# Kernel tuning notes

Hardware: AMD Instinct MI355X
Metric: run time of the kernel (lower is better)

Reference implementation:

```python
import jax, jax.numpy as jnp
import numpy as np

N, P, E, D, OUT = 4096, 2048, 65536, 1024, 128


def _lin(k, fin, fout):
    kw, kb = jax.random.split(k)
    s = 1.0 / np.sqrt(fin)
    return (jax.random.uniform(kw, (fin, fout), jnp.float32, -s, s),
            jax.random.uniform(kb, (fout,), jnp.float32, -s, s))


def setup_inputs() -> dict:
    key = jax.random.key(0)
    ks = jax.random.split(key, 16)
    inst_feat = jax.random.normal(ks[0], (N, D), jnp.float32)
    phra_feat = jax.random.normal(ks[1], (P, D), jnp.float32)
    # unique (subject, object) pairs: the original overwrites duplicates in connection_marker
    pair_ids = jax.random.choice(ks[2], N * N, (E,), replace=False)
    conn_mat = jnp.stack([pair_ids // N, pair_ids % N]).astype(jnp.int32)  # [2, E]
    # every phrase id appears -> exist_phra_id == arange(P), matching original indexing
    phra_clu_idx = jax.random.permutation(ks[3], jnp.arange(E, dtype=jnp.int32) % P)
    p_s_W, p_s_b = _lin(ks[4], 2 * D, OUT)
    s_p_W, s_p_b = _lin(ks[5], 2 * D, OUT)
    p_o_W, p_o_b = _lin(ks[6], 2 * D, OUT)
    o_p_W, o_p_b = _lin(ks[7], 2 * D, OUT)
    inst_w1_W, inst_w1_b = _lin(ks[8], D, D)
    inst_w2_W, inst_w2_b = _lin(ks[9], D, D)
    phra_w1_W, phra_w1_b = _lin(ks[10], D, D)
    phra_w2_W, phra_w2_b = _lin(ks[11], D, D)
    return dict(inst_feat=inst_feat, phra_feat=phra_feat, conn_mat=conn_mat,
                phra_clu_idx=phra_clu_idx,
                p_s_W=p_s_W, p_s_b=p_s_b, p_o_W=p_o_W, p_o_b=p_o_b,
                o_p_W=o_p_W, o_p_b=o_p_b, s_p_W=s_p_W, s_p_b=s_p_b,
                inst_w1_W=inst_w1_W, inst_w1_b=inst_w1_b,
                inst_w2_W=inst_w2_W, inst_w2_b=inst_w2_b,
                phra_w1_W=phra_w1_W, phra_w1_b=phra_w1_b,
                phra_w2_W=phra_w2_W, phra_w2_b=phra_w2_b)


def _gated_msg(src, tgt, W, b):
    # MassageGenerator: gate = sigmoid(relu([src; tgt] @ W + b)).mean(1); msg = src * gate
    gate = jax.nn.sigmoid(jax.nn.relu(jnp.concatenate([src, tgt], axis=1) @ W + b)).mean(axis=1)
    return src * gate[:, None]


def _seg_mean(x, seg, num_segments):
    s = jax.ops.segment_sum(x, seg, num_segments=num_segments)
    c = jax.ops.segment_sum(jnp.ones((x.shape[0],), x.dtype), seg, num_segments=num_segments)
    return s / jnp.maximum(c, 1.0)[:, None]  # zeros where no edges == padded msg


def _refine(msg, tar, w1_W, w1_b, w2_W, w2_b):
    # MassageApply: out = input1 + relu(w1(input1)) + relu(w2(input2)); input1 = summed msg
    return msg + jax.nn.relu(msg @ w1_W + w1_b) + jax.nn.relu(tar @ w2_W + w2_b)


def reference(inst_feat, phra_feat, conn_mat, phra_clu_idx,
              p_s_W, p_s_b, p_o_W, p_o_b, o_p_W, o_p_b, s_p_W, s_p_b,
              inst_w1_W, inst_w1_b, inst_w2_W, inst_w2_b,
              phra_w1_W, phra_w1_b, phra_w2_W, phra_w2_b):
    s_idx, o_idx = conn_mat[0], conn_mat[1]
    subj_f = inst_feat[s_idx]          # [E, D]
    obj_f = inst_feat[o_idx]           # [E, D]
    phr_f = phra_feat[phra_clu_idx]    # [E, D]
    n, p = inst_feat.shape[0], phra_feat.shape[0]
    # phrase -> subject / object messages, mean over each node's incident edges
    p_s = _seg_mean(_gated_msg(phr_f, subj_f, p_s_W, p_s_b), s_idx, n)
    p_o = _seg_mean(_gated_msg(phr_f, obj_f, p_o_W, p_o_b), o_idx, n)
    # object / subject -> phrase messages, mean over edges sharing a cluster id
    o_p = _seg_mean(_gated_msg(obj_f, phr_f, o_p_W, o_p_b), phra_clu_idx, p)
    s_p = _seg_mean(_gated_msg(subj_f, phr_f, s_p_W, s_p_b), phra_clu_idx, p)
    inst_out = _refine((p_o + p_s) * 0.5, inst_feat, inst_w1_W, inst_w1_b, inst_w2_W, inst_w2_b)
    phra_out = _refine((o_p + s_p) * 0.5, phra_feat, phra_w1_W, phra_w1_b, phra_w2_W, phra_w2_b)
    return inst_out, phra_out
```

## Files before the change

### kernel.cpp

```cpp
#include <hip/hip_runtime.h>
#include <math.h>

constexpr int NN  = 4096;
constexpr int PP  = 2048;
constexpr int EE  = 65536;
constexpr int DD  = 1024;
constexpr int OUTF = 128;
constexpr int G4  = 512;

typedef __attribute__((ext_vector_type(8))) short short8v;
typedef __attribute__((ext_vector_type(4))) float f32x4;

__device__ __forceinline__ float sigmoid_relu(float z) {
    z = fmaxf(z, 0.0f);
    return 1.0f / (1.0f + __expf(-z));
}
__device__ __forceinline__ float b2f(ushort u) {
    return __uint_as_float(((unsigned int)u) << 16);
}
__device__ __forceinline__ ushort f2b(float f) {
    unsigned int x = __float_as_uint(f);
    return (ushort)((x + 0x7fffu + ((x >> 16) & 1u)) >> 16);
}
__device__ __forceinline__ unsigned int pack2(float a, float b) {
    return (unsigned int)f2b(a) | ((unsigned int)f2b(b) << 16);
}
__device__ __forceinline__ float lo16(unsigned int u) { return __uint_as_float(u << 16); }
__device__ __forceinline__ float hi16(unsigned int u) { return __uint_as_float(u & 0xffff0000u); }

#define GLD16(gptr, lptr) \
    __builtin_amdgcn_global_load_lds((__attribute__((address_space(1))) const void*)(gptr), \
                                     (__attribute__((address_space(3))) void*)(lptr), 16, 0, 0)
#define ASM_VMCNT(n) asm volatile("s_waitcnt vmcnt(" #n ")" ::: "memory")
#define BARRIER() do { asm volatile("" ::: "memory"); \
                       __builtin_amdgcn_s_barrier();  \
                       asm volatile("" ::: "memory"); } while (0)

constexpr int NCNT    = 2 * (NN + NN + PP);
constexpr int NB_ZERO = NCNT / 256;
constexpr int NB_F2B  = (NN + PP) * DD / 4 / 256;
constexpr int NB_PACK = G4 * DD / 256;
constexpr int NB_WT   = 4 * (DD / 64) * (DD / 64);

__global__ __launch_bounds__(256) void prep_kernel(
        int* __restrict__ cntBlock,
        const float* __restrict__ instF, const float* __restrict__ phraF,
        ushort* __restrict__ instB, ushort* __restrict__ phraB,
        const float* __restrict__ psW, const float* __restrict__ poW,
        const float* __restrict__ opW, const float* __restrict__ spW,
        const float* __restrict__ psB, const float* __restrict__ poB,
        const float* __restrict__ opB, const float* __restrict__ spB,
        ushort* __restrict__ WiT, ushort* __restrict__ WpT,
        float* __restrict__ biascat,
        const float* __restrict__ W0, const float* __restrict__ W1,
        const float* __restrict__ W2, const float* __restrict__ W3,
        ushort* __restrict__ T0, ushort* __restrict__ T1,
        ushort* __restrict__ T2, ushort* __restrict__ T3) {
    __shared__ float tile[64][65];
    int b = blockIdx.x, t = threadIdx.x;
    if (b < NB_ZERO) {
        cntBlock[b * 256 + t] = 0;
        return;
    }
    b -= NB_ZERO;
    if (b < NB_F2B) {
        int i = b * 256 + t;
        constexpr int na4 = NN * DD / 4;
        if (i < na4) {
            float4 v = ((const float4*)instF)[i];
            ushort4 u; u.x = f2b(v.x); u.y = f2b(v.y); u.z = f2b(v.z); u.w = f2b(v.w);
            ((ushort4*)instB)[i] = u;
        } else {
            int j = i - na4;
            float4 v = ((const float4*)phraF)[j];
            ushort4 u; u.x = f2b(v.x); u.y = f2b(v.y); u.z = f2b(v.z); u.w = f2b(v.w);
            ((ushort4*)phraB)[j] = u;
        }
        return;
    }
    b -= NB_F2B;
    if (b < NB_PACK) {
        int idx = b * 256 + t;
        int n = idx >> 10, k = idx & 1023;
        int g = n >> 7, j = n & 127;
        float wi, wp;
        if (g == 0)      { wi = psW[(size_t)(DD + k) * OUTF + j]; wp = psW[(size_t)k * OUTF + j]; }
        else if (g == 1) { wi = poW[(size_t)(DD + k) * OUTF + j]; wp = poW[(size_t)k * OUTF + j]; }
        else if (g == 2) { wi = opW[(size_t)k * OUTF + j];        wp = opW[(size_t)(DD + k) * OUTF + j]; }
        else             { wi = spW[(size_t)k * OUTF + j];        wp = spW[(size_t)(DD + k) * OUTF + j]; }
        WiT[idx] = f2b(wi);
        WpT[idx] = f2b(wp);
        if (idx < G4) {
            int gg = idx >> 7, jj = idx & 127;
            biascat[idx] = (gg == 0) ? psB[jj] : (gg == 1) ? poB[jj]
                         : (gg == 2) ? opB[jj] : spB[jj];
        }
        return;
    }
    b -= NB_PACK;
    int z = b >> 8, rest = b & 255;
    const float* W = (z == 0) ? W0 : (z == 1) ? W1 : (z == 2) ? W2 : W3;
    ushort*      T = (z == 0) ? T0 : (z == 1) ? T1 : (z == 2) ? T2 : T3;
    int k0 = (rest & 15) * 64, n0 = (rest >> 4) * 64;
    int tx = t & 63, ty = t >> 6;
    #pragma unroll
    for (int i = 0; i < 64; i += 4)
        tile[ty + i][tx] = W[(size_t)(k0 + ty + i) * DD + n0 + tx];
    __syncthreads();
    #pragma unroll
    for (int i = 0; i < 64; i += 4)
        T[(size_t)(n0 + ty + i) * DD + k0 + tx] = f2b(tile[tx][ty + i]);
}

template<int BROWS>
__device__ __forceinline__ void stage_tiles(const ushort* __restrict__ A,
                                            const ushort* __restrict__ BT,
                                            int bm, int bn, int k0,
                                            ushort* Asl, ushort* Bsl, int t) {
    #pragma unroll
    for (int r = 0; r < 4; r++) {
        int ch = r * 256 + t;
        int row = ch >> 3;
        int sw = ((ch & 7) ^ (row & 7)) << 3;
        GLD16(A + (size_t)(bm + row) * DD + k0 + sw, &Asl[ch * 8]);
    }
    #pragma unroll
    for (int r = 0; r < BROWS / 32; r++) {
        int ch = r * 256 + t;
        int row = ch >> 3;
        int sw = ((ch & 7) ^ (row & 7)) << 3;
        GLD16(BT + (size_t)(bn + row) * DD + k0 + sw, &Bsl[ch * 8]);
    }
}

template<int NACC>
__device__ __forceinline__ void compute_tiles(const ushort* Asl, const ushort* Bsl,
                                              f32x4 (&acc)[4][NACC],
                                              int wr, int wc, int lr, int lk) {
    #pragma unroll
    for (int kk = 0; kk < 2; kk++) {
        int ch16 = kk * 4 + lk;
        short8v a[4], b[NACC];
        #pragma unroll
        for (int m = 0; m < 4; m++) {
            int ra = wr + m * 16 + lr;
            a[m] = *(const short8v*)&Asl[ra * 64 + ((ch16 ^ (ra & 7)) << 3)];
        }
        #pragma unroll
        for (int n = 0; n < NACC; n++) {
            int rb = wc + n * 16 + lr;
            b[n] = *(const short8v*)&Bsl[rb * 64 + ((ch16 ^ (rb & 7)) << 3)];
        }
        #pragma unroll
        for (int m = 0; m < 4; m++)
            #pragma unroll
            for (int n = 0; n < NACC; n++)
                acc[m][n] = __builtin_amdgcn_mfma_f32_16x16x32_bf16(a[m], b[n], acc[m][n], 0, 0, 0);
    }
}

__global__ __launch_bounds__(256) void mfma_tables_kernel(
        const ushort* __restrict__ instB, const ushort* __restrict__ WiT,
        const ushort* __restrict__ phraB, const ushort* __restrict__ WpT,
        const float* __restrict__ biascat,
        ushort* __restrict__ TiB, ushort* __restrict__ TpB) {
    __shared__ ushort Asl[2][128 * 64];
    __shared__ ushort Bsl[2][64 * 64];
    int bx = blockIdx.x;
    const ushort *A, *BT; ushort* C; const float* bias;
    if (bx < NN / 128) { A = instB; BT = WiT; C = TiB; bias = nullptr; }
    else { bx -= NN / 128; A = phraB; BT = WpT; C = TpB; bias = biascat; }
    int bm = bx * 128, bn = blockIdx.y * 64;
    int t = threadIdx.x;
    const int lane = t & 63, w = t >> 6;
    const int wr = (w >> 1) * 64, wc = (w & 1) * 32;
    const int lr = lane & 15, lk = lane >> 4;
    f32x4 acc[4][2] = {};

    int cur = 0;
    stage_tiles<64>(A, BT, bm, bn, 0, Asl[0], Bsl[0], t);
    for (int k0 = 0; k0 < DD; k0 += 64) {
        int nxt = cur ^ 1;
        if (k0 + 64 < DD) {
            stage_tiles<64>(A, BT, bm, bn, k0 + 64, Asl[nxt], Bsl[nxt], t);
            ASM_VMCNT(6);
        } else {
            ASM_VMCNT(0);
        }
        BARRIER();
        compute_tiles<2>(Asl[cur], Bsl[cur], acc, wr, wc, lr, lk);
        BARRIER();
        cur = nxt;
    }
    #pragma unroll
    for (int m = 0; m < 4; m++) {
        int row = bm + wr + m * 16 + lk * 4;
        #pragma unroll
        for (int n = 0; n < 2; n++) {
            int col = bn + wc + n * 16 + lr;
            float bv = bias ? bias[col] : 0.f;
            #pragma unroll
            for (int r = 0; r < 4; r++)
                C[(size_t)(row + r) * G4 + col] = f2b(acc[m][n][r] + bv);
        }
    }
}

__global__ __launch_bounds__(256) void mfma_refine_kernel(
        const ushort* __restrict__ imsgB, const ushort* __restrict__ instB,
        const ushort* __restrict__ iw1T, const ushort* __restrict__ iw2T,
        const float* __restrict__ ib1, const float* __restrict__ ib2,
        float* __restrict__ iout,
        const ushort* __restrict__ pmsgB, const ushort* __restrict__ phraB,
        const ushort* __restrict__ pw1T, const ushort* __restrict__ pw2T,
        const float* __restrict__ pb1, const float* __restrict__ pb2,
        float* __restrict__ pout) {
    __shared__ ushort Asl[2][128 * 64];
    __shared__ ushort Bsl[2][64 * 64];
    int bx = blockIdx.x;
    const ushort *Am, *Af, *W1, *W2; const float *b1, *b2; float* out;
    if (bx < NN / 128) {
        Am = imsgB; Af = instB; W1 = iw1T; W2 = iw2T; b1 = ib1; b2 = ib2; out = iout;
    } else {
        bx -= NN / 128;
        Am = pmsgB; Af = phraB; W1 = pw1T; W2 = pw2T; b1 = pb1; b2 = pb2; out = pout;
    }
    int bm = bx * 128, bn = blockIdx.y * 64;
    int t = threadIdx.x;
    const int lane = t & 63, w = t >> 6;
    const int wr = (w >> 1) * 64, wc = (w & 1) * 32;
    const int lr = lane & 15, lk = lane >> 4;
    f32x4 acc1[4][2] = {};
    f32x4 acc2[4][2] = {};

    int cur = 0;
    stage_tiles<64>(Am, W1, bm, bn, 0, Asl[0], Bsl[0], t);
    auto run = [&](const ushort* A, const ushort* B, f32x4 (&acc)[4][2],
                   const ushort* An, const ushort* Bn) {
        for (int k0 = 0; k0 < DD; k0 += 64) {
            int nxt = cur ^ 1;
            if (k0 + 64 < DD) {
                stage_tiles<64>(A, B, bm, bn, k0 + 64, Asl[nxt], Bsl[nxt], t);
                ASM_VMCNT(6);
            } else if (An) {
                stage_tiles<64>(An, Bn, bm, bn, 0, Asl[nxt], Bsl[nxt], t);
                ASM_VMCNT(6);
            } else {
                ASM_VMCNT(0);
            }
            BARRIER();
            compute_tiles<2>(Asl[cur], Bsl[cur], acc, wr, wc, lr, lk);
            BARRIER();
            cur = nxt;
        }
    };
    run(Am, W1, acc1, Af, W2);
    run(Af, W2, acc2, nullptr, nullptr);

    #pragma unroll
    for (int m = 0; m < 4; m++) {
        int row = bm + wr + m * 16 + lk * 4;
        #pragma unroll
        for (int n = 0; n < 2; n++) {
            int col = bn + wc + n * 16 + lr;
            float vb1 = b1[col], vb2 = b2[col];
            #pragma unroll
            for (int r = 0; r < 4; r++) {
                float v = b2f(Am[(size_t)(row + r) * DD + col])
                        + fmaxf(acc1[m][n][r] + vb1, 0.f)
                        + fmaxf(acc2[m][n][r] + vb2, 0.f);
                out[(size_t)(row + r) * DD + col] = v;
            }
        }
    }
}

__global__ void hist_kernel(const int* __restrict__ s_idx, const int* __restrict__ o_idx,
                            const int* __restrict__ c_idx,
                            int* cntS, int* cntO, int* cntC) {
    int e = blockIdx.x * blockDim.x + threadIdx.x;
    if (e >= EE) return;
    atomicAdd(&cntS[s_idx[e]], 1);
    atomicAdd(&cntO[o_idx[e]], 1);
    atomicAdd(&cntC[c_idx[e]], 1);
}

__global__ __launch_bounds__(1024) void scan3_kernel(
        const int* __restrict__ cntS, const int* __restrict__ cntO,
        const int* __restrict__ cntC,
        int* __restrict__ startS, int* __restrict__ startO, int* __restrict__ startC) {
    const int* cnt; int* start; int n;
    if (blockIdx.x == 0)      { cnt = cntS; start = startS; n = NN; }
    else if (blockIdx.x == 1) { cnt = cntO; start = startO; n = NN; }
    else                      { cnt = cntC; start = startC; n = PP; }
    __shared__ int sh[1024];
    int t = threadIdx.x;
    int per = n >> 10;
    int base = t * per;
    int s = 0;
    for (int i = 0; i < per; i++) s += cnt[base + i];
    sh[t] = s;
    __syncthreads();
    for (int off = 1; off < 1024; off <<= 1) {
        int v = (t >= off) ? sh[t - off] : 0;
        __syncthreads();
        sh[t] += v;
        __syncthreads();
    }
    int ex = (t == 0) ? 0 : sh[t - 1];
    for (int i = 0; i < per; i++) { start[base + i] = ex; ex += cnt[base + i]; }
    if (t == 1023) start[n] = ex;
}

__global__ __launch_bounds__(256) void gate_kernel(
        const int* __restrict__ s_idx, const int* __restrict__ o_idx,
        const int* __restrict__ c_idx,
        const int* __restrict__ startS, const int* __restrict__ startO,
        const int* __restrict__ startC,
        int* __restrict__ curS, int* __restrict__ curO, int* __restrict__ curC,
        const ushort* __restrict__ Ti, const ushort* __restrict__ Tp,
        int2* __restrict__ pkS, int2* __restrict__ pkO, int4* __restrict__ pkC) {
    int gid = blockIdx.x * 256 + threadIdx.x;
    int e = gid >> 6, lane = gid & 63;
    if (e >= EE) return;
    int s = s_idx[e], o = o_idx[e], c = c_idx[e];
    const unsigned int* tpc = (const unsigned int*)(Tp + (size_t)c * G4);
    const unsigned int* tis = (const unsigned int*)(Ti + (size_t)s * G4);
    const unsigned int* tio = (const unsigned int*)(Ti + (size_t)o * G4);
    auto pairSig = [](unsigned int a, unsigned int b) {
        float lo = __uint_as_float(a << 16) + __uint_as_float(b << 16);
        float hi = __uint_as_float(a & 0xffff0000u) + __uint_as_float(b & 0xffff0000u);
        return sigmoid_relu(lo) + sigmoid_relu(hi);
    };
    float s0 = pairSig(tpc[lane],       tis[lane]);
    float s1 = pairSig(tpc[64 + lane],  tio[64 + lane]);
    float s2 = pairSig(tpc[128 + lane], tio[128 + lane]);
    float s3 = pairSig(tpc[192 + lane], tis[192 + lane]);
    #pragma unroll
    for (int off = 32; off; off >>= 1) {
        s0 += __shfl_xor(s0, off);
        s1 += __shfl_xor(s1, off);
        s2 += __shfl_xor(s2, off);
        s3 += __shfl_xor(s3, off);
    }
    if (lane == 0) {
        const float inv = 1.0f / 128.0f;
        int ps = startS[s] + atomicAdd(&curS[s], 1);
        int po = startO[o] + atomicAdd(&curO[o], 1);
        int pc = startC[c] + atomicAdd(&curC[c], 1);
        pkS[ps] = make_int2(c, __float_as_int(s0 * inv));
        pkO[po] = make_int2(c, __float_as_int(s1 * inv));
        pkC[pc] = make_int4(o, s, __float_as_int(s2 * inv), __float_as_int(s3 * inv));
    }
}

__device__ __forceinline__ void acc8(float* a, uint4 v, float g) {
    a[0] += g * lo16(v.x); a[1] += g * hi16(v.x);
    a[2] += g * lo16(v.y); a[3] += g * hi16(v.y);
    a[4] += g * lo16(v.z); a[5] += g * hi16(v.z);
    a[6] += g * lo16(v.w); a[7] += g * hi16(v.w);
}

__global__ __launch_bounds__(256) void seg_kernel(
        const ushort* __restrict__ phraB, const ushort* __restrict__ instB,
        const int2* __restrict__ pkS, const int* __restrict__ startS,
        const int2* __restrict__ pkO, const int* __restrict__ startO,
        const int4* __restrict__ pkC, const int* __restrict__ startC,
        ushort* __restrict__ imsgB, ushort* __restrict__ pmsgB) {
    __shared__ float lds[4][32 * 9];
    int bid = blockIdx.x;
    int x = bid & 7;
    int q = x >> 1;
    int sub = ((bid >> 3) << 1) + (x & 1);
    int qoff = q * 256;
    int w = threadIdx.x >> 6, lane = threadIdx.x & 63;
    int half = lane >> 5, l32 = lane & 31;
    float a[8];
    #pragma unroll
    for (int k = 0; k < 8; k++) a[k] = 0.f;
    bool instSide = sub < NN / 2;
    int lenScale;
    ushort* msgB;
    int base2;
    if (instSide) {
        int node = sub * 2 + (w >> 1);
        const int2* pk_list = (w & 1) ? pkO : pkS;
        const int*  start   = (w & 1) ? startO : startS;
        int b = start[node], e = start[node + 1];
        lenScale = e - b;
        for (int base = b; base < e; base += 64) {
            int n = min(64, e - base);
            int2 pkv = pk_list[base + min(lane, n - 1)];
            int   c0 = __shfl(pkv.x, 0);
            int   c1 = __shfl(pkv.x, 1 < n ? 1 : 0);
            float g0 = __int_as_float(__shfl(pkv.y, 0));
            float g1 = (1 < n) ? __int_as_float(__shfl(pkv.y, 1)) : 0.f;
            int   myc = half ? c1 : c0;
            float myg = half ? g1 : g0;
            uint4 v = *(const uint4*)(phraB + (size_t)myc * DD + qoff + l32 * 8);
            for (int j = 2; j < n; j += 2) {
                int   d0 = __shfl(pkv.x, j);
                int   d1 = __shfl(pkv.x, j + 1 < n ? j + 1 : j);
                float h0 = __int_as_float(__shfl(pkv.y, j));
                float h1 = (j + 1 < n) ? __int_as_float(__shfl(pkv.y, j + 1)) : 0.f;
                int   nc = half ? d1 : d0;
                float ng = half ? h1 : h0;
                uint4 vn = *(const uint4*)(phraB + (size_t)nc * DD + qoff + l32 * 8);
                acc8(a, v, myg);
                v = vn; myg = ng;
            }
            acc8(a, v, myg);
        }
        msgB = imsgB; base2 = sub * 2;
    } else {
        int pbx = sub - NN / 2;
        int p = pbx * 2 + (w >> 1);
        int cb = startC[p], ce = startC[p + 1];
        lenScale = ce - cb;
        int mid = cb + ((ce - cb) >> 1);
        int mb = (w & 1) ? mid : cb;
        int me = (w & 1) ? ce : mid;
        for (int base = mb; base < me; base += 64) {
            int n = min(64, me - base);
            int4 pkv = pkC[base + min(lane, n - 1)];
            int   o0  = __shfl(pkv.x, 0);
            int   o1  = __shfl(pkv.x, 1 < n ? 1 : 0);
            int   si0 = __shfl(pkv.y, 0);
            int   si1 = __shfl(pkv.y, 1 < n ? 1 : 0);
            float go0 = __int_as_float(__shfl(pkv.z, 0));
            float go1 = (1 < n) ? __int_as_float(__shfl(pkv.z, 1)) : 0.f;
            float gs0 = __int_as_float(__shfl(pkv.w, 0));
            float gs1 = (1 < n) ? __int_as_float(__shfl(pkv.w, 1)) : 0.f;
            int   myo = half ? o1 : o0,  mys = half ? si1 : si0;
            float mygo = half ? go1 : go0, mygs = half ? gs1 : gs0;
            uint4 vo = *(const uint4*)(instB + (size_t)myo * DD + qoff + l32 * 8);
            uint4 vs = *(const uint4*)(instB + (size_t)mys * DD + qoff + l32 * 8);
            for (int j = 2; j < n; j += 2) {
                int   no0  = __shfl(pkv.x, j);
                int   no1  = __shfl(pkv.x, j + 1 < n ? j + 1 : j);
                int   ns0  = __shfl(pkv.y, j);
                int   ns1  = __shfl(pkv.y, j + 1 < n ? j + 1 : j);
                float ngo0 = __int_as_float(__shfl(pkv.z, j));
                float ngo1 = (j + 1 < n) ? __int_as_float(__shfl(pkv.z, j + 1)) : 0.f;
                float ngs0 = __int_as_float(__shfl(pkv.w, j));
                float ngs1 = (j + 1 < n) ? __int_as_float(__shfl(pkv.w, j + 1)) : 0.f;
                int   nno = half ? no1 : no0,  nns = half ? ns1 : ns0;
                float ngo = half ? ngo1 : ngo0, ngs = half ? ngs1 : ngs0;
                uint4 vno = *(const uint4*)(instB + (size_t)nno * DD + qoff + l32 * 8);
                uint4 vns = *(const uint4*)(instB + (size_t)nns * DD + qoff + l32 * 8);
                acc8(a, vo, mygo);
                acc8(a, vs, mygs);
                vo = vno; vs = vns; mygo = ngo; mygs = ngs;
            }
            acc8(a, vo, mygo);
            acc8(a, vs, mygs);
        }
        msgB = pmsgB; base2 = pbx * 2;
    }
    #pragma unroll
    for (int k = 0; k < 8; k++) a[k] += __shfl_xor(a[k], 32);
    float scale = 0.5f / (float)max(lenScale, 1);
    if (half == 0) {
        #pragma unroll
        for (int k = 0; k < 8; k++) lds[w][l32 * 9 + k] = a[k] * scale;
    }
    __syncthreads();
    if (threadIdx.x < 64) {
        int nodeSel = threadIdx.x >> 5;
        int l = threadIdx.x & 31;
        int w0 = nodeSel * 2;
        float s0 = lds[w0][l * 9 + 0] + lds[w0 + 1][l * 9 + 0];
        float s1 = lds[w0][l * 9 + 1] + lds[w0 + 1][l * 9 + 1];
        float s2 = lds[w0][l * 9 + 2] + lds[w0 + 1][l * 9 + 2];
        float s3 = lds[w0][l * 9 + 3] + lds[w0 + 1][l * 9 + 3];
        float s4 = lds[w0][l * 9 + 4] + lds[w0 + 1][l * 9 + 4];
        float s5 = lds[w0][l * 9 + 5] + lds[w0 + 1][l * 9 + 5];
        float s6 = lds[w0][l * 9 + 6] + lds[w0 + 1][l * 9 + 6];
        float s7 = lds[w0][l * 9 + 7] + lds[w0 + 1][l * 9 + 7];
        uint4 o;
        o.x = pack2(s0, s1);
        o.y = pack2(s2, s3);
        o.z = pack2(s4, s5);
        o.w = pack2(s6, s7);
        *(uint4*)&msgB[(size_t)(base2 + nodeSel) * DD + qoff + l * 8] = o;
    }
}

extern "C" void kernel_launch(void* const* d_in, const int* in_sizes, int n_in,
                              void* d_out, int out_size, void* d_ws, size_t ws_size,
                              hipStream_t stream) {
    (void)in_sizes; (void)n_in; (void)out_size; (void)ws_size;
    const float* inst_feat = (const float*)d_in[0];
    const float* phra_feat = (const float*)d_in[1];
    const int*   conn      = (const int*)d_in[2];
    const int*   clu       = (const int*)d_in[3];
    const float* psW = (const float*)d_in[4];  const float* psB = (const float*)d_in[5];
    const float* poW = (const float*)d_in[6];  const float* poB = (const float*)d_in[7];
    const float* opW = (const float*)d_in[8];  const float* opB = (const float*)d_in[9];
    const float* spW = (const float*)d_in[10]; const float* spB = (const float*)d_in[11];
    const float* iw1W = (const float*)d_in[12]; const float* iw1B = (const float*)d_in[13];
    const float* iw2W = (const float*)d_in[14]; const float* iw2B = (const float*)d_in[15];
    const float* pw1W = (const float*)d_in[16]; const float* pw1B = (const float*)d_in[17];
    const float* pw2W = (const float*)d_in[18]; const float* pw2B = (const float*)d_in[19];
    const int* s_idx = conn;
    const int* o_idx = conn + EE;

    char* ws = (char*)d_ws;
    size_t off = 0;
    auto alloc = [&](size_t bytes) {
        char* p = ws + off;
        off += (bytes + 255) & ~(size_t)255;
        return p;
    };
    ushort* instB = (ushort*)alloc((size_t)NN * DD * 2);
    ushort* phraB = (ushort*)alloc((size_t)PP * DD * 2);
    ushort* WiT   = (ushort*)alloc((size_t)G4 * DD * 2);
    ushort* WpT   = (ushort*)alloc((size_t)G4 * DD * 2);
    ushort* iw1T  = (ushort*)alloc((size_t)DD * DD * 2);
    ushort* iw2T  = (ushort*)alloc((size_t)DD * DD * 2);
    ushort* pw1T  = (ushort*)alloc((size_t)DD * DD * 2);
    ushort* pw2T  = (ushort*)alloc((size_t)DD * DD * 2);
    float* biascat = (float*)alloc(G4 * 4);
    ushort* TiB   = (ushort*)alloc((size_t)NN * G4 * 2);
    ushort* TpB   = (ushort*)alloc((size_t)PP * G4 * 2);
    int* cntBlock = (int*)alloc((size_t)NCNT * 4);
    int* cntS = cntBlock;      int* cntO = cntS + NN;  int* cntC = cntO + NN;
    int* curS = cntC + PP;     int* curO = curS + NN;  int* curC = curO + NN;
    int* startS = (int*)alloc((NN + 1) * 4);
    int* startO = (int*)alloc((NN + 1) * 4);
    int* startC = (int*)alloc((PP + 1) * 4);
    int2* pkS   = (int2*)alloc((size_t)EE * 8);
    int2* pkO   = (int2*)alloc((size_t)EE * 8);
    int4* pkC   = (int4*)alloc((size_t)EE * 16);
    ushort* imsgB = (ushort*)alloc((size_t)NN * DD * 2);
    ushort* pmsgB = (ushort*)alloc((size_t)PP * DD * 2);

    float* inst_out = (float*)d_out;
    float* phra_out = inst_out + (size_t)NN * DD;

    prep_kernel<<<NB_ZERO + NB_F2B + NB_PACK + NB_WT, 256, 0, stream>>>(
        cntBlock, inst_feat, phra_feat, instB, phraB,
        psW, poW, opW, spW, psB, poB, opB, spB, WiT, WpT, biascat,
        iw1W, iw2W, pw1W, pw2W, iw1T, iw2T, pw1T, pw2T);

    hist_kernel<<<EE / 256, 256, 0, stream>>>(s_idx, o_idx, clu, cntS, cntO, cntC);
    scan3_kernel<<<3, 1024, 0, stream>>>(cntS, cntO, cntC, startS, startO, startC);

    mfma_tables_kernel<<<dim3((NN + PP) / 128, G4 / 64), 256, 0, stream>>>(
        instB, WiT, phraB, WpT, biascat, TiB, TpB);

    gate_kernel<<<(EE * 64) / 256, 256, 0, stream>>>(
        s_idx, o_idx, clu, startS, startO, startC, curS, curO, curC,
        TiB, TpB, pkS, pkO, pkC);

    seg_kernel<<<(NN / 2 + PP / 2) * 4, 256, 0, stream>>>(
        phraB, instB, pkS, startS, pkO, startO, pkC, startC, imsgB, pmsgB);

    mfma_refine_kernel<<<dim3((NN + PP) / 128, DD / 64), 256, 0, stream>>>(
        imsgB, instB, iw1T, iw2T, iw1B, iw2B, inst_out,
        pmsgB, phraB, pw1T, pw2T, pw1B, pw2B, phra_out);
}
```

Baseline: 148.3 us.

## Triple-buffer MFMA GEMM pipelines and split gate computation with precomputed scatter positions

Both MFMA GEMM kernels move from a double-buffered K loop with two barriers per step to a three-stage LDS ring with one barrier per step. The refine kernel's two chained GEMMs become a single 32-step loop. This is meant to cut barrier stalls and keep two tiles of loads in flight, at the cost of 50% more shared memory per block, which may lower occupancy. Scatter positions are now computed by a separate scatter kernel. The gate kernel spreads each edge's four gate reductions across four waves, so each wave does one reduction. This trades more blocks and extra position arrays for removing the atomics from the gate path.

```diff
diff --git a/kernel.cpp b/kernel.cpp
--- a/kernel.cpp
+++ b/kernel.cpp
@@ -164,8 +164,8 @@
         const ushort* __restrict__ phraB, const ushort* __restrict__ WpT,
         const float* __restrict__ biascat,
         ushort* __restrict__ TiB, ushort* __restrict__ TpB) {
-    __shared__ ushort Asl[2][128 * 64];
-    __shared__ ushort Bsl[2][64 * 64];
+    __shared__ ushort Asl[3][128 * 64];
+    __shared__ ushort Bsl[3][64 * 64];
     int bx = blockIdx.x;
     const ushort *A, *BT; ushort* C; const float* bias;
     if (bx < NN / 128) { A = instB; BT = WiT; C = TiB; bias = nullptr; }
@@ -177,20 +177,14 @@
     const int lr = lane & 15, lk = lane >> 4;
     f32x4 acc[4][2] = {};
 
-    int cur = 0;
     stage_tiles<64>(A, BT, bm, bn, 0, Asl[0], Bsl[0], t);
-    for (int k0 = 0; k0 < DD; k0 += 64) {
-        int nxt = cur ^ 1;
-        if (k0 + 64 < DD) {
-            stage_tiles<64>(A, BT, bm, bn, k0 + 64, Asl[nxt], Bsl[nxt], t);
-            ASM_VMCNT(6);
-        } else {
-            ASM_VMCNT(0);
-        }
+    stage_tiles<64>(A, BT, bm, bn, 64, Asl[1], Bsl[1], t);
+    for (int s = 0; s < 16; s++) {
+        if (s == 15) { ASM_VMCNT(0); } else { ASM_VMCNT(6); }
         BARRIER();
-        compute_tiles<2>(Asl[cur], Bsl[cur], acc, wr, wc, lr, lk);
-        BARRIER();
-        cur = nxt;
+        compute_tiles<2>(Asl[s % 3], Bsl[s % 3], acc, wr, wc, lr, lk);
+        if (s + 2 < 16)
+            stage_tiles<64>(A, BT, bm, bn, (s + 2) * 64, Asl[(s + 2) % 3], Bsl[(s + 2) % 3], t);
     }
     #pragma unroll
     for (int m = 0; m < 4; m++) {
@@ -215,8 +209,8 @@
         const ushort* __restrict__ pw1T, const ushort* __restrict__ pw2T,
         const float* __restrict__ pb1, const float* __restrict__ pb2,
         float* __restrict__ pout) {
-    __shared__ ushort Asl[2][128 * 64];
-    __shared__ ushort Bsl[2][64 * 64];
+    __shared__ ushort Asl[3][128 * 64];
+    __shared__ ushort Bsl[3][64 * 64];
     int bx = blockIdx.x;
     const ushort *Am, *Af, *W1, *W2; const float *b1, *b2; float* out;
     if (bx < NN / 128) {
@@ -233,29 +227,21 @@
     f32x4 acc1[4][2] = {};
     f32x4 acc2[4][2] = {};
 
-    int cur = 0;
-    stage_tiles<64>(Am, W1, bm, bn, 0, Asl[0], Bsl[0], t);
-    auto run = [&](const ushort* A, const ushort* B, f32x4 (&acc)[4][2],
-                   const ushort* An, const ushort* Bn) {
-        for (int k0 = 0; k0 < DD; k0 += 64) {
-            int nxt = cur ^ 1;
-            if (k0 + 64 < DD) {
-                stage_tiles<64>(A, B, bm, bn, k0 + 64, Asl[nxt], Bsl[nxt], t);
-                ASM_VMCNT(6);
-            } else if (An) {
-                stage_tiles<64>(An, Bn, bm, bn, 0, Asl[nxt], Bsl[nxt], t);
-                ASM_VMCNT(6);
-            } else {
-                ASM_VMCNT(0);
-            }
-            BARRIER();
-            compute_tiles<2>(Asl[cur], Bsl[cur], acc, wr, wc, lr, lk);
-            BARRIER();
-            cur = nxt;
-        }
+    auto stageStep = [&](int s) {
+        if (s < 16)      stage_tiles<64>(Am, W1, bm, bn, s * 64,
+                                         Asl[s % 3], Bsl[s % 3], t);
+        else if (s < 32) stage_tiles<64>(Af, W2, bm, bn, (s - 16) * 64,
+                                         Asl[s % 3], Bsl[s % 3], t);
     };
-    run(Am, W1, acc1, Af, W2);
-    run(Af, W2, acc2, nullptr, nullptr);
+    stageStep(0);
+    stageStep(1);
+    for (int s = 0; s < 32; s++) {
+        if (s == 31) { ASM_VMCNT(0); } else { ASM_VMCNT(6); }
+        BARRIER();
+        if (s < 16) compute_tiles<2>(Asl[s % 3], Bsl[s % 3], acc1, wr, wc, lr, lk);
+        else        compute_tiles<2>(Asl[s % 3], Bsl[s % 3], acc2, wr, wc, lr, lk);
+        stageStep(s + 2);
+    }
 
     #pragma unroll
     for (int m = 0; m < 4; m++) {
@@ -312,45 +298,55 @@
     if (t == 1023) start[n] = ex;
 }
 
+__global__ void scatter_kernel(const int* __restrict__ s_idx, const int* __restrict__ o_idx,
+                               const int* __restrict__ c_idx,
+                               const int* __restrict__ startS, const int* __restrict__ startO,
+                               const int* __restrict__ startC,
+                               int* curS, int* curO, int* curC,
+                               int* posS, int* posO, int* posC) {
+    int e = blockIdx.x * blockDim.x + threadIdx.x;
+    if (e >= EE) return;
+    posS[e] = startS[s_idx[e]] + atomicAdd(&curS[s_idx[e]], 1);
+    posO[e] = startO[o_idx[e]] + atomicAdd(&curO[o_idx[e]], 1);
+    posC[e] = startC[c_idx[e]] + atomicAdd(&curC[c_idx[e]], 1);
+}
+
 __global__ __launch_bounds__(256) void gate_kernel(
         const int* __restrict__ s_idx, const int* __restrict__ o_idx,
         const int* __restrict__ c_idx,
-        const int* __restrict__ startS, const int* __restrict__ startO,
-        const int* __restrict__ startC,
-        int* __restrict__ curS, int* __restrict__ curO, int* __restrict__ curC,
+        const int* __restrict__ posS, const int* __restrict__ posO,
+        const int* __restrict__ posC,
         const ushort* __restrict__ Ti, const ushort* __restrict__ Tp,
         int2* __restrict__ pkS, int2* __restrict__ pkO, int4* __restrict__ pkC) {
-    int gid = blockIdx.x * 256 + threadIdx.x;
-    int e = gid >> 6, lane = gid & 63;
-    if (e >= EE) return;
-    int s = s_idx[e], o = o_idx[e], c = c_idx[e];
-    const unsigned int* tpc = (const unsigned int*)(Tp + (size_t)c * G4);
-    const unsigned int* tis = (const unsigned int*)(Ti + (size_t)s * G4);
-    const unsigned int* tio = (const unsigned int*)(Ti + (size_t)o * G4);
-    auto pairSig = [](unsigned int a, unsigned int b) {
-        float lo = __uint_as_float(a << 16) + __uint_as_float(b << 16);
-        float hi = __uint_as_float(a & 0xffff0000u) + __uint_as_float(b & 0xffff0000u);
-        return sigmoid_relu(lo) + sigmoid_relu(hi);
-    };
-    float s0 = pairSig(tpc[lane],       tis[lane]);
-    float s1 = pairSig(tpc[64 + lane],  tio[64 + lane]);
-    float s2 = pairSig(tpc[128 + lane], tio[128 + lane]);
-    float s3 = pairSig(tpc[192 + lane], tis[192 + lane]);
-    #pragma unroll
-    for (int off = 32; off; off >>= 1) {
-        s0 += __shfl_xor(s0, off);
-        s1 += __shfl_xor(s1, off);
-        s2 += __shfl_xor(s2, off);
-        s3 += __shfl_xor(s3, off);
-    }
+    int bid = blockIdx.x;
+    int x = bid & 7;
+    int q = x >> 1;
+    int subB = ((bid >> 3) << 1) + (x & 1);
+    int w = threadIdx.x >> 6, lane = threadIdx.x & 63;
+    int e = subB * 4 + w;
+    int c = c_idx[e];
+    int partner = (q == 0 || q == 3) ? s_idx[e] : o_idx[e];
+    const unsigned int* tpc = (const unsigned int*)(Tp + (size_t)c * G4) + q * 64;
+    const unsigned int* tix = (const unsigned int*)(Ti + (size_t)partner * G4) + q * 64;
+    unsigned int a = tpc[lane], bb = tix[lane];
+    float lo = __uint_as_float(a << 16) + __uint_as_float(bb << 16);
+    float hi = __uint_as_float(a & 0xffff0000u) + __uint_as_float(bb & 0xffff0000u);
+    float s = sigmoid_relu(lo) + sigmoid_relu(hi);
+    #pragma unroll
+    for (int off = 32; off; off >>= 1) s += __shfl_xor(s, off);
     if (lane == 0) {
-        const float inv = 1.0f / 128.0f;
-        int ps = startS[s] + atomicAdd(&curS[s], 1);
-        int po = startO[o] + atomicAdd(&curO[o], 1);
-        int pc = startC[c] + atomicAdd(&curC[c], 1);
-        pkS[ps] = make_int2(c, __float_as_int(s0 * inv));
-        pkO[po] = make_int2(c, __float_as_int(s1 * inv));
-        pkC[pc] = make_int4(o, s, __float_as_int(s2 * inv), __float_as_int(s3 * inv));
+        float g = s * (1.0f / 128.0f);
+        if (q == 0) {
+            pkS[posS[e]] = make_int2(c, __float_as_int(g));
+        } else if (q == 1) {
+            pkO[posO[e]] = make_int2(c, __float_as_int(g));
+        } else if (q == 2) {
+            int* p = (int*)&pkC[posC[e]];
+            *(int2*)p = make_int2(o_idx[e], s_idx[e]);
+            p[2] = __float_as_int(g);
+        } else {
+            ((int*)&pkC[posC[e]])[3] = __float_as_int(g);
+        }
     }
 }
 
@@ -529,6 +525,9 @@
     int* startS = (int*)alloc((NN + 1) * 4);
     int* startO = (int*)alloc((NN + 1) * 4);
     int* startC = (int*)alloc((PP + 1) * 4);
+    int* posS   = (int*)alloc((size_t)EE * 4);
+    int* posO   = (int*)alloc((size_t)EE * 4);
+    int* posC   = (int*)alloc((size_t)EE * 4);
     int2* pkS   = (int2*)alloc((size_t)EE * 8);
     int2* pkO   = (int2*)alloc((size_t)EE * 8);
     int4* pkC   = (int4*)alloc((size_t)EE * 16);
@@ -545,13 +544,14 @@
 
     hist_kernel<<<EE / 256, 256, 0, stream>>>(s_idx, o_idx, clu, cntS, cntO, cntC);
     scan3_kernel<<<3, 1024, 0, stream>>>(cntS, cntO, cntC, startS, startO, startC);
+    scatter_kernel<<<EE / 256, 256, 0, stream>>>(s_idx, o_idx, clu, startS, startO, startC,
+                                                 curS, curO, curC, posS, posO, posC);
 
     mfma_tables_kernel<<<dim3((NN + PP) / 128, G4 / 64), 256, 0, stream>>>(
         instB, WiT, phraB, WpT, biascat, TiB, TpB);
 
-    gate_kernel<<<(EE * 64) / 256, 256, 0, stream>>>(
-        s_idx, o_idx, clu, startS, startO, startC, curS, curO, curC,
-        TiB, TpB, pkS, pkO, pkC);
+    gate_kernel<<<EE, 256, 0, stream>>>(
+        s_idx, o_idx, clu, posS, posO, posC, TiB, TpB, pkS, pkO, pkC);
 
     seg_kernel<<<(NN / 2 + PP / 2) * 4, 256, 0, stream>>>(
         phraB, instB, pkS, startS, pkO, startO, pkC, startC, imsgB, pmsgB);
```

New measurement: 198.3 us. +33.7%, slower.
